# Kernel tuning notes

Measured on AMD Instinct MI355X. Metric: run time of the kernel, lower is better.

## Reference

```python
import jax, jax.numpy as jnp
import numpy as np
import math

WS = 8          # window size
DIM = 32        # per-head dim
NH = 8          # num_head
TH = 16         # total_head
B, H, W = 4, 128, 128
WA = WS * WS    # window area


def _rel_pos_index():
    coords = np.stack(np.meshgrid(np.arange(WS), np.arange(WS), indexing='ij'))  # (2, WS, WS)
    cf = coords.reshape(2, -1)                      # (2, WA)
    rc = cf[:, :, None] - cf[:, None, :]            # (2, WA, WA)
    rc = rc.transpose(1, 2, 0).copy()               # (WA, WA, 2)
    rc[:, :, 0] += WS - 1
    rc[:, :, 1] += WS - 1
    rc[:, :, 0] *= 2 * WS - 1
    return rc.sum(-1)                               # (WA, WA)


def setup_inputs() -> dict:
    key = jax.random.key(0)
    k1, k2, k3, k4 = jax.random.split(key, 4)
    qkv = jax.random.normal(k1, (B, NH, 3 * DIM, H, W), dtype=jnp.float32)
    ch = jax.random.normal(k2, (B, (TH - NH) * DIM, H, W), dtype=jnp.float32)
    logit_scale = jnp.log(10.0) * jnp.ones((NH, 1, 1), dtype=jnp.float32)
    rel_bias_table = 0.02 * jax.random.normal(k3, ((2 * WS - 1) ** 2, NH), dtype=jnp.float32)
    proj_w = 0.02 * jax.random.normal(k4, (NH * DIM, NH * DIM), dtype=jnp.float32)  # 1x1 conv
    proj_b = jnp.zeros((NH * DIM,), dtype=jnp.float32)
    rel_index = jnp.asarray(_rel_pos_index(), dtype=jnp.int32)
    return {"qkv": qkv, "ch": ch, "logit_scale": logit_scale,
            "rel_bias_table": rel_bias_table, "proj_w": proj_w,
            "proj_b": proj_b, "rel_index": rel_index}


def _window_partition(x):
    # x: (B, l, c, H, W) -> (B*nh*nw, l, WA, c)
    b, l, c, h, w = x.shape
    nh, nw = h // WS, w // WS
    x = x.reshape(b, l, c, nh, WS, nw, WS)
    x = x.transpose(0, 3, 5, 1, 4, 6, 2)            # b, nh, nw, l, wh, ww, c
    return x.reshape(b * nh * nw, l, WA, c)


def _l2norm(x):
    n = jnp.sqrt(jnp.sum(x * x, axis=-1, keepdims=True))
    return x / jnp.maximum(n, 1e-12)


def reference(qkv, ch, logit_scale, rel_bias_table, proj_w, proj_b, rel_index):
    b, L, C3, h, w = qkv.shape
    nh, nw = h // WS, w // WS
    qkvw = _window_partition(qkv)                   # (Bw, L, WA, 3*DIM)
    q, k, v = jnp.split(qkvw, 3, axis=-1)           # each (Bw, L, WA, DIM)

    # helper gating
    lch = TH - NH
    chw = _window_partition(ch.reshape(b, lch, DIM, h, w))  # (Bw, lch, WA, DIM)
    chm = jnp.mean(chw, axis=1, keepdims=True)      # (Bw, 1, WA, DIM)
    v = v * chm

    # cosine attention
    attn = jnp.einsum('wlqc,wlkc->wlqk', _l2norm(q), _l2norm(k))
    scale = jnp.exp(jnp.minimum(logit_scale, math.log(1.0 / 0.01)))  # (L,1,1)
    bias = rel_bias_table[rel_index.reshape(-1)].reshape(WA, WA, NH)
    bias = bias.transpose(2, 0, 1)[None]            # (1, L, WA, WA)
    attn = jax.nn.softmax(attn * scale[None] + bias, axis=-1)
    x = jnp.einsum('wlqk,wlkc->wlqc', attn, v)      # (Bw, L, WA, DIM)

    # window unpartition -> (B, L*DIM, H, W)
    x = x.reshape(b, nh, nw, L, WS, WS, DIM)
    x = x.transpose(0, 3, 6, 1, 4, 2, 5)            # b, l, c, nh, wh, nw, ww
    x = x.reshape(b, L * DIM, h, w)

    # 1x1 conv projection
    x = jnp.einsum('bchw,oc->bohw', x, proj_w) + proj_b[None, :, None, None]
    return x
```

## Files before the change

### kernel.cpp

```cpp
#include <hip/hip_runtime.h>


typedef __attribute__((ext_vector_type(8))) short short8v;
typedef __attribute__((ext_vector_type(4))) float f32x4;
typedef __attribute__((ext_vector_type(2))) unsigned int u32x2;

#define PLANE 16384

static __device__ __forceinline__ unsigned short f2bf(float x) {
  union { float f; unsigned u; } v; v.f = x;
  unsigned r = v.u + 0x7fff + ((v.u >> 16) & 1);
  return (unsigned short)(r >> 16);
}
static __device__ __forceinline__ float bf2f(unsigned short b) {
  union { unsigned u; float f; } v; v.u = ((unsigned)b) << 16;
  return v.f;
}

__global__ __launch_bounds__(256) void prep_kernel(
    const float* __restrict__ btab, const int* __restrict__ ridx,
    const float* __restrict__ pw, float* __restrict__ biasG,
    unsigned int* __restrict__ wbf)
{
  const int blk = blockIdx.x, tid = threadIdx.x;
  if (blk < 128) {
    int i = blk * 256 + tid;
    int h = i >> 12, qk = i & 4095;
    biasG[i] = btab[ridx[qk] * 8 + h];
  } else {
    int i = (blk - 128) * 256 + tid;
    wbf[i] = (unsigned)f2bf(pw[2 * i]) | ((unsigned)f2bf(pw[2 * i + 1]) << 16);
  }
}

__global__ __launch_bounds__(512, 4) void fused_kernel(
    const float* __restrict__ qkv, const float* __restrict__ ch,
    const float* __restrict__ lsc, const float* __restrict__ biasG,
    const unsigned short* __restrict__ wbf, const float* __restrict__ pb,
    float* __restrict__ out)
{
  __shared__ __align__(16) char smem[65536];
  float* chm = (float*)smem;

  const int tid = threadIdx.x;
  int bid = blockIdx.x;
  bid = (bid & 7) * 64 + (bid >> 3);
  const int b   = bid >> 7;
  const int wy  = (bid >> 3) & 15;
  const int wxp = bid & 7;
  const int y0  = wy << 3, x0 = wxp << 4;

  const int h = tid >> 6, lane = tid & 63;
  const int lg = lane >> 4, lr = lane & 15;

  {
    const float* cb = ch + ((size_t)(b * 256)) * PLANE;
#pragma unroll
    for (int t = 0; t < 2; ++t) {
      int idx = tid + t * 512;
      int c = idx >> 5, row = (idx >> 2) & 7, xq = idx & 3;
      const float4* src = (const float4*)(cb + (size_t)c * PLANE
                                          + (y0 + row) * 128 + x0) + xq;
      float4 a = {0.f, 0.f, 0.f, 0.f};
#pragma unroll
      for (int l = 0; l < 8; ++l) {
        float4 tv = src[(size_t)(l * 32) * (PLANE / 4)];
        a.x += tv.x; a.y += tv.y; a.z += tv.z; a.w += tv.w;
      }
      a.x *= 0.125f; a.y *= 0.125f; a.z *= 0.125f; a.w *= 0.125f;
      *(float4*)(chm + 132 * c + 16 * row + 4 * xq) = a;
    }
  }
  __syncthreads();

  const size_t qbase = ((size_t)((b * 8 + h) * 96)) * PLANE;
  const float* qg = qkv + qbase;
  const float* kg = qg + (size_t)32 * PLANE;
  const float* vg = qg + (size_t)64 * PLANE;
  const float scale = __expf(fminf(lsc[h], 4.6051701859880914f));

  short8v vf[2][2][2];
#pragma unroll
  for (int win = 0; win < 2; ++win) {
    const int xw = x0 + win * 8;
#pragma unroll
    for (int dt = 0; dt < 2; ++dt) {
      const int d = 16 * dt + lr;
      const float* vp = vg + (size_t)d * PLANE;
      const float* cm = chm + 132 * d;
#pragma unroll
      for (int m = 0; m < 2; ++m) {
        int ka = 4 * lg + 32 * m, kb2 = ka + 16;
        int ra = ka >> 3, ca = ka & 7, rb = kb2 >> 3, cb2 = kb2 & 7;
        float4 va  = *(const float4*)(vp + (y0 + ra) * 128 + xw + ca);
        float4 vb  = *(const float4*)(vp + (y0 + rb) * 128 + xw + cb2);
        f32x4 caf = *(const f32x4*)(cm + 16 * ra + 8 * win + ca);
        f32x4 cbf = *(const f32x4*)(cm + 16 * rb + 8 * win + cb2);
        vf[win][dt][m][0] = (short)f2bf(va.x * caf[0]);
        vf[win][dt][m][1] = (short)f2bf(va.y * caf[1]);
        vf[win][dt][m][2] = (short)f2bf(va.z * caf[2]);
        vf[win][dt][m][3] = (short)f2bf(va.w * caf[3]);
        vf[win][dt][m][4] = (short)f2bf(vb.x * cbf[0]);
        vf[win][dt][m][5] = (short)f2bf(vb.y * cbf[1]);
        vf[win][dt][m][6] = (short)f2bf(vb.z * cbf[2]);
        vf[win][dt][m][7] = (short)f2bf(vb.w * cbf[3]);
      }
    }
  }
  __syncthreads();

  const float* bgh = biasG + (h << 12);

#pragma unroll 1
  for (int win = 0; win < 2; ++win) {
    const int xw = x0 + win * 8;

    short8v khi[4], klo[4];
#pragma unroll
    for (int kt = 0; kt < 4; ++kt) {
      int kpos = 16 * kt + lr;
      int spk = (y0 + (kpos >> 3)) * 128 + xw + (kpos & 7);
      float kk[8], nr = 0.f;
#pragma unroll
      for (int j = 0; j < 8; ++j) {
        kk[j] = kg[(size_t)(8 * lg + j) * PLANE + spk];
        nr = fmaf(kk[j], kk[j], nr);
      }
      nr += __shfl_xor(nr, 16);
      nr += __shfl_xor(nr, 32);
      float iv = 1.f / fmaxf(sqrtf(nr), 1e-12f);
#pragma unroll
      for (int j = 0; j < 8; ++j) {
        float x = kk[j] * iv;
        unsigned short hb = f2bf(x);
        khi[kt][j] = (short)hb;
        klo[kt][j] = (short)f2bf(x - bf2f(hb));
      }
    }

#pragma unroll 1
    for (int st = 0; st < 4; ++st) {
      int q = 16 * st + lr;
      int spq = (y0 + (q >> 3)) * 128 + xw + (q & 7);
      float qq[8], nrq = 0.f;
#pragma unroll
      for (int j = 0; j < 8; ++j) {
        qq[j] = qg[(size_t)(8 * lg + j) * PLANE + spq];
        nrq = fmaf(qq[j], qq[j], nrq);
      }
      nrq += __shfl_xor(nrq, 16);
      nrq += __shfl_xor(nrq, 32);
      const float fq = scale / fmaxf(sqrtf(nrq), 1e-12f);

      short8v qhi, qlo;
#pragma unroll
      for (int j = 0; j < 8; ++j) {
        float x = qq[j] * fq;
        unsigned short hb = f2bf(x);
        qhi[j] = (short)hb;
        qlo[j] = (short)f2bf(x - bf2f(hb));
      }

      const float4* bq = (const float4*)(bgh + (q << 6));
      float e[16], mx = -1e30f;
#pragma unroll
      for (int kt = 0; kt < 4; ++kt) {
        f32x4 a = {0.f, 0.f, 0.f, 0.f};
        a = __builtin_amdgcn_mfma_f32_16x16x32_bf16(klo[kt], qhi, a, 0, 0, 0);
        a = __builtin_amdgcn_mfma_f32_16x16x32_bf16(khi[kt], qlo, a, 0, 0, 0);
        a = __builtin_amdgcn_mfma_f32_16x16x32_bf16(khi[kt], qhi, a, 0, 0, 0);
        float4 b4 = bq[4 * kt + lg];
        float bb[4] = {b4.x, b4.y, b4.z, b4.w};
#pragma unroll
        for (int r = 0; r < 4; ++r) {
          float lv = a[r] + bb[r];
          e[4 * kt + r] = lv;
          mx = fmaxf(mx, lv);
        }
      }
      mx = fmaxf(mx, __shfl_xor(mx, 16));
      mx = fmaxf(mx, __shfl_xor(mx, 32));
      float s = 0.f;
#pragma unroll
      for (int i = 0; i < 16; ++i) { e[i] = __expf(e[i] - mx); s += e[i]; }
      s += __shfl_xor(s, 16);
      s += __shfl_xor(s, 32);
      float rl = 1.f / s;

      short8v pf[2];
#pragma unroll
      for (int m = 0; m < 2; ++m)
#pragma unroll
        for (int j = 0; j < 8; ++j)
          pf[m][j] = (short)f2bf(e[4 * (j >> 2) + 8 * m + (j & 3)]);

      int pl = ((q >> 3) << 4) + win * 8 + (q & 7);
#pragma unroll
      for (int dt = 0; dt < 2; ++dt) {
        f32x4 o = {0.f, 0.f, 0.f, 0.f};
        o = __builtin_amdgcn_mfma_f32_16x16x32_bf16(vf[win][dt][0], pf[0], o, 0, 0, 0);
        o = __builtin_amdgcn_mfma_f32_16x16x32_bf16(vf[win][dt][1], pf[1], o, 0, 0, 0);
        u32x2 ww;
        ww[0] = (unsigned)f2bf(o[0] * rl) | ((unsigned)f2bf(o[1] * rl) << 16);
        ww[1] = (unsigned)f2bf(o[2] * rl) | ((unsigned)f2bf(o[3] * rl) << 16);
        unsigned off = (unsigned)(pl * 512)
                     + (((unsigned)(64 * h + 32 * dt + 8 * lg)) ^ ((unsigned)(pl & 7) << 4));
        *(u32x2*)(smem + off) = ww;
      }
    }
  }
  __syncthreads();

  f32x4 acc[2][8];
#pragma unroll
  for (int i = 0; i < 2; ++i)
#pragma unroll
    for (int j = 0; j < 8; ++j) acc[i][j] = (f32x4){0.f, 0.f, 0.f, 0.f};

#pragma unroll 1
  for (int kc = 0; kc < 8; ++kc) {
    short8v wf0 = *(const short8v*)(wbf + (size_t)(32 * h + lr) * 256 + 32 * kc + 8 * lg);
    short8v wf1 = *(const short8v*)(wbf + (size_t)(32 * h + 16 + lr) * 256 + 32 * kc + 8 * lg);
    short8v xf[8];
#pragma unroll
    for (int pt = 0; pt < 8; ++pt) {
      int pl = 16 * pt + lr;
      unsigned off = (unsigned)(pl * 512)
                   + (((unsigned)(64 * kc + 16 * lg)) ^ ((unsigned)(pl & 7) << 4));
      xf[pt] = *(const short8v*)(smem + off);
    }
#pragma unroll
    for (int pt = 0; pt < 8; ++pt) {
      acc[0][pt] = __builtin_amdgcn_mfma_f32_16x16x32_bf16(wf0, xf[pt], acc[0][pt], 0, 0, 0);
      acc[1][pt] = __builtin_amdgcn_mfma_f32_16x16x32_bf16(wf1, xf[pt], acc[1][pt], 0, 0, 0);
    }
  }

#pragma unroll
  for (int ot = 0; ot < 2; ++ot) {
#pragma unroll
    for (int r = 0; r < 4; ++r) {
      int o = 32 * h + 16 * ot + 4 * lg + r;
      float bv = pb[o];
      float* op = out + ((size_t)(b * 256 + o)) * PLANE;
#pragma unroll
      for (int pt = 0; pt < 8; ++pt)
        op[(y0 + pt) * 128 + x0 + lr] = acc[ot][pt][r] + bv;
    }
  }
}

extern "C" void kernel_launch(void* const* d_in, const int* in_sizes, int n_in,
                              void* d_out, int out_size, void* d_ws, size_t ws_size,
                              hipStream_t stream) {
  const float* qkv  = (const float*)d_in[0];
  const float* ch   = (const float*)d_in[1];
  const float* lsc  = (const float*)d_in[2];
  const float* btab = (const float*)d_in[3];
  const float* pw   = (const float*)d_in[4];
  const float* pb   = (const float*)d_in[5];
  const int*   ridx = (const int*)d_in[6];
  float* out = (float*)d_out;

  char* ws = (char*)d_ws;
  float*          biasG = (float*)ws;
  unsigned short* wbf   = (unsigned short*)(ws + 131072);

  prep_kernel<<<dim3(256), dim3(256), 0, stream>>>(btab, ridx, pw,
                                                   biasG, (unsigned int*)wbf);
  fused_kernel<<<dim3(512), dim3(512), 0, stream>>>(qkv, ch, lsc, biasG,
                                                    wbf, pb, out);
}
```

Baseline: 130.8 us.

## Remap waves to window/query tiles, loop heads with LDS-staged K and prefetch

Waves are reassigned from one attention head each to one (window, query-tile) pair each, and every wave now loops over all 8 heads. Each head's K tile is staged once per block into LDS as a bf16 hi/lo split, and the next head's K is prefetched into registers while the current head is processed. L2 normalisation of q and k is moved to a scale applied to the MFMA output instead of being applied to the inputs. The trade is two extra barriers per head, a larger LDS footprint, and four waves each reloading the same V and bias data, with slightly different rounding.

```diff
diff --git a/kernel.cpp b/kernel.cpp
--- a/kernel.cpp
+++ b/kernel.cpp
@@ -6,6 +6,7 @@
 typedef __attribute__((ext_vector_type(2))) unsigned int u32x2;
 
 #define PLANE 16384
+#define LOG100 4.6051701859880914f
 
 static __device__ __forceinline__ unsigned short f2bf(float x) {
   union { float f; unsigned u; } v; v.f = x;
@@ -39,8 +40,10 @@
     const unsigned short* __restrict__ wbf, const float* __restrict__ pb,
     float* __restrict__ out)
 {
-  __shared__ __align__(16) char smem[65536];
+  __shared__ __align__(16) char smem[81920];
   float* chm = (float*)smem;
+  unsigned short* sKhi = (unsigned short*)(smem + 65536);
+  unsigned short* sKlo = (unsigned short*)(smem + 73728);
 
   const int tid = threadIdx.x;
   int bid = blockIdx.x;
@@ -50,8 +53,10 @@
   const int wxp = bid & 7;
   const int y0  = wy << 3, x0 = wxp << 4;
 
-  const int h = tid >> 6, lane = tid & 63;
+  const int wv = tid >> 6, lane = tid & 63;
   const int lg = lane >> 4, lr = lane & 15;
+  const int win = wv >> 2, st = wv & 3;
+  const int xw  = x0 + win * 8;
 
   {
     const float* cb = ch + ((size_t)(b * 256)) * PLANE;
@@ -73,143 +78,171 @@
   }
   __syncthreads();
 
-  const size_t qbase = ((size_t)((b * 8 + h) * 96)) * PLANE;
-  const float* qg = qkv + qbase;
-  const float* kg = qg + (size_t)32 * PLANE;
-  const float* vg = qg + (size_t)64 * PLANE;
-  const float scale = __expf(fminf(lsc[h], 4.6051701859880914f));
-
-  short8v vf[2][2][2];
-#pragma unroll
-  for (int win = 0; win < 2; ++win) {
-    const int xw = x0 + win * 8;
+  unsigned cpk[2][2][4];
+#pragma unroll
+  for (int dt = 0; dt < 2; ++dt) {
+    const float* cm = chm + 132 * (16 * dt + lr);
+#pragma unroll
+    for (int m = 0; m < 2; ++m) {
+      int ka = 4 * lg + 32 * m, kb = ka + 16;
+      int pa = 16 * (ka >> 3) + 8 * win + (ka & 7);
+      int pb2 = 16 * (kb >> 3) + 8 * win + (kb & 7);
+      f32x4 ca = *(const f32x4*)(cm + pa);
+      f32x4 cb2 = *(const f32x4*)(cm + pb2);
+      cpk[dt][m][0] = (unsigned)f2bf(ca[0]) | ((unsigned)f2bf(ca[1]) << 16);
+      cpk[dt][m][1] = (unsigned)f2bf(ca[2]) | ((unsigned)f2bf(ca[3]) << 16);
+      cpk[dt][m][2] = (unsigned)f2bf(cb2[0]) | ((unsigned)f2bf(cb2[1]) << 16);
+      cpk[dt][m][3] = (unsigned)f2bf(cb2[2]) | ((unsigned)f2bf(cb2[3]) << 16);
+    }
+  }
+  __syncthreads();
+
+  const int sq4 = tid & 3;
+  const int sdd = ((tid >> 2) & 15) | ((tid >> 8) << 4);
+  const int sr2 = (tid >> 6) & 3;
+  const int sgo1 = (y0 + sr2) * 128 + x0 + 4 * sq4;
+  const int sgo2 = (y0 + sr2 + 4) * 128 + x0 + 4 * sq4;
+  const int sp1 = 16 * sr2 + 4 * sq4;
+  const int sp2 = 16 * (sr2 + 4) + 4 * sq4;
+
+  const size_t qkv0 = ((size_t)(b * 8) * 96) * PLANE;
+  const float* kg0 = qkv + qkv0 + (size_t)(32 + sdd) * PLANE;
+
+  float4 f1 = *(const float4*)(kg0 + sgo1);
+  float4 f2 = *(const float4*)(kg0 + sgo2);
+
+#pragma unroll 1
+  for (int h = 0; h < 8; ++h) {
+    {
+#define STG(val, pos_) { unsigned short hb_ = f2bf(val);                     \
+        sKhi[32 * (pos_) + sdd] = hb_;                                       \
+        sKlo[32 * (pos_) + sdd] = f2bf((val) - bf2f(hb_)); }
+      STG(f1.x, sp1 + 0) STG(f1.y, sp1 + 1) STG(f1.z, sp1 + 2) STG(f1.w, sp1 + 3)
+      STG(f2.x, sp2 + 0) STG(f2.y, sp2 + 1) STG(f2.z, sp2 + 2) STG(f2.w, sp2 + 3)
+#undef STG
+    }
+    __syncthreads();
+
+    if (h < 7) {
+      const float* kgn = qkv + qkv0 + (size_t)((h + 1) * 96 + 32 + sdd) * PLANE;
+      f1 = *(const float4*)(kgn + sgo1);
+      f2 = *(const float4*)(kgn + sgo2);
+    }
+
+    const float* qg = qkv + qkv0 + (size_t)(h * 96) * PLANE;
+    const float* vg = qg + (size_t)64 * PLANE;
+    const float scale = __expf(fminf(lsc[h], LOG100));
+    const int q = 16 * st + lr;
+    const int spq = (y0 + (q >> 3)) * 128 + xw + (q & 7);
+
+    float qq[8];
+#pragma unroll
+    for (int j = 0; j < 8; ++j)
+      qq[j] = qg[(size_t)(8 * lg + j) * PLANE + spq];
+
+    short8v vf[2][2];
 #pragma unroll
     for (int dt = 0; dt < 2; ++dt) {
-      const int d = 16 * dt + lr;
-      const float* vp = vg + (size_t)d * PLANE;
-      const float* cm = chm + 132 * d;
+      const float* vp = vg + (size_t)(16 * dt + lr) * PLANE;
 #pragma unroll
       for (int m = 0; m < 2; ++m) {
-        int ka = 4 * lg + 32 * m, kb2 = ka + 16;
-        int ra = ka >> 3, ca = ka & 7, rb = kb2 >> 3, cb2 = kb2 & 7;
-        float4 va  = *(const float4*)(vp + (y0 + ra) * 128 + xw + ca);
-        float4 vb  = *(const float4*)(vp + (y0 + rb) * 128 + xw + cb2);
-        f32x4 caf = *(const f32x4*)(cm + 16 * ra + 8 * win + ca);
-        f32x4 cbf = *(const f32x4*)(cm + 16 * rb + 8 * win + cb2);
-        vf[win][dt][m][0] = (short)f2bf(va.x * caf[0]);
-        vf[win][dt][m][1] = (short)f2bf(va.y * caf[1]);
-        vf[win][dt][m][2] = (short)f2bf(va.z * caf[2]);
-        vf[win][dt][m][3] = (short)f2bf(va.w * caf[3]);
-        vf[win][dt][m][4] = (short)f2bf(vb.x * cbf[0]);
-        vf[win][dt][m][5] = (short)f2bf(vb.y * cbf[1]);
-        vf[win][dt][m][6] = (short)f2bf(vb.z * cbf[2]);
-        vf[win][dt][m][7] = (short)f2bf(vb.w * cbf[3]);
+        int ka = 4 * lg + 32 * m, kb = ka + 16;
+        float4 va = *(const float4*)(vp + (y0 + (ka >> 3)) * 128 + xw + (ka & 7));
+        float4 vb = *(const float4*)(vp + (y0 + (kb >> 3)) * 128 + xw + (kb & 7));
+        const unsigned* cp = cpk[dt][m];
+        vf[dt][m][0] = (short)f2bf(va.x * bf2f((unsigned short)(cp[0] & 0xffff)));
+        vf[dt][m][1] = (short)f2bf(va.y * bf2f((unsigned short)(cp[0] >> 16)));
+        vf[dt][m][2] = (short)f2bf(va.z * bf2f((unsigned short)(cp[1] & 0xffff)));
+        vf[dt][m][3] = (short)f2bf(va.w * bf2f((unsigned short)(cp[1] >> 16)));
+        vf[dt][m][4] = (short)f2bf(vb.x * bf2f((unsigned short)(cp[2] & 0xffff)));
+        vf[dt][m][5] = (short)f2bf(vb.y * bf2f((unsigned short)(cp[2] >> 16)));
+        vf[dt][m][6] = (short)f2bf(vb.z * bf2f((unsigned short)(cp[3] & 0xffff)));
+        vf[dt][m][7] = (short)f2bf(vb.w * bf2f((unsigned short)(cp[3] >> 16)));
       }
     }
-  }
-  __syncthreads();
-
-  const float* bgh = biasG + (h << 12);
-
-#pragma unroll 1
-  for (int win = 0; win < 2; ++win) {
-    const int xw = x0 + win * 8;
 
     short8v khi[4], klo[4];
+    float ivk[4];
 #pragma unroll
     for (int kt = 0; kt < 4; ++kt) {
-      int kpos = 16 * kt + lr;
-      int spk = (y0 + (kpos >> 3)) * 128 + xw + (kpos & 7);
-      float kk[8], nr = 0.f;
+      int pp = 16 * (2 * kt + (lr >> 3)) + 8 * win + (lr & 7);
+      khi[kt] = *(const short8v*)(sKhi + 32 * pp + 8 * lg);
+      klo[kt] = *(const short8v*)(sKlo + 32 * pp + 8 * lg);
+      float nr = 0.f;
 #pragma unroll
       for (int j = 0; j < 8; ++j) {
-        kk[j] = kg[(size_t)(8 * lg + j) * PLANE + spk];
-        nr = fmaf(kk[j], kk[j], nr);
+        float kr = bf2f((unsigned short)khi[kt][j]) + bf2f((unsigned short)klo[kt][j]);
+        nr = fmaf(kr, kr, nr);
       }
       nr += __shfl_xor(nr, 16);
       nr += __shfl_xor(nr, 32);
-      float iv = 1.f / fmaxf(sqrtf(nr), 1e-12f);
-#pragma unroll
-      for (int j = 0; j < 8; ++j) {
-        float x = kk[j] * iv;
-        unsigned short hb = f2bf(x);
-        khi[kt][j] = (short)hb;
-        klo[kt][j] = (short)f2bf(x - bf2f(hb));
+      ivk[kt] = 1.f / fmaxf(sqrtf(nr), 1e-12f);
+    }
+
+    float nrq = 0.f;
+#pragma unroll
+    for (int j = 0; j < 8; ++j) nrq = fmaf(qq[j], qq[j], nrq);
+    nrq += __shfl_xor(nrq, 16);
+    nrq += __shfl_xor(nrq, 32);
+    const float fq = scale / fmaxf(sqrtf(nrq), 1e-12f);
+
+    short8v qhi, qlo;
+#pragma unroll
+    for (int j = 0; j < 8; ++j) {
+      unsigned short hb = f2bf(qq[j]);
+      qhi[j] = (short)hb;
+      qlo[j] = (short)f2bf(qq[j] - bf2f(hb));
+    }
+
+    const float4* bq = (const float4*)(biasG + (h << 12) + (q << 6));
+    float e[16], mx = -1e30f;
+#pragma unroll
+    for (int kt = 0; kt < 4; ++kt) {
+      f32x4 a = {0.f, 0.f, 0.f, 0.f};
+      a = __builtin_amdgcn_mfma_f32_16x16x32_bf16(klo[kt], qhi, a, 0, 0, 0);
+      a = __builtin_amdgcn_mfma_f32_16x16x32_bf16(khi[kt], qlo, a, 0, 0, 0);
+      a = __builtin_amdgcn_mfma_f32_16x16x32_bf16(khi[kt], qhi, a, 0, 0, 0);
+      float4 b4 = bq[4 * kt + lg];
+      float bb[4] = {b4.x, b4.y, b4.z, b4.w};
+#pragma unroll
+      for (int r = 0; r < 4; ++r) {
+        float fkr = __shfl(ivk[kt], 4 * lg + r);
+        float lv = a[r] * (fq * fkr) + bb[r];
+        e[4 * kt + r] = lv;
+        mx = fmaxf(mx, lv);
       }
     }
-
-#pragma unroll 1
-    for (int st = 0; st < 4; ++st) {
-      int q = 16 * st + lr;
-      int spq = (y0 + (q >> 3)) * 128 + xw + (q & 7);
-      float qq[8], nrq = 0.f;
-#pragma unroll
-      for (int j = 0; j < 8; ++j) {
-        qq[j] = qg[(size_t)(8 * lg + j) * PLANE + spq];
-        nrq = fmaf(qq[j], qq[j], nrq);
-      }
-      nrq += __shfl_xor(nrq, 16);
-      nrq += __shfl_xor(nrq, 32);
-      const float fq = scale / fmaxf(sqrtf(nrq), 1e-12f);
-
-      short8v qhi, qlo;
-#pragma unroll
-      for (int j = 0; j < 8; ++j) {
-        float x = qq[j] * fq;
-        unsigned short hb = f2bf(x);
-        qhi[j] = (short)hb;
-        qlo[j] = (short)f2bf(x - bf2f(hb));
-      }
-
-      const float4* bq = (const float4*)(bgh + (q << 6));
-      float e[16], mx = -1e30f;
-#pragma unroll
-      for (int kt = 0; kt < 4; ++kt) {
-        f32x4 a = {0.f, 0.f, 0.f, 0.f};
-        a = __builtin_amdgcn_mfma_f32_16x16x32_bf16(klo[kt], qhi, a, 0, 0, 0);
-        a = __builtin_amdgcn_mfma_f32_16x16x32_bf16(khi[kt], qlo, a, 0, 0, 0);
-        a = __builtin_amdgcn_mfma_f32_16x16x32_bf16(khi[kt], qhi, a, 0, 0, 0);
-        float4 b4 = bq[4 * kt + lg];
-        float bb[4] = {b4.x, b4.y, b4.z, b4.w};
-#pragma unroll
-        for (int r = 0; r < 4; ++r) {
-          float lv = a[r] + bb[r];
-          e[4 * kt + r] = lv;
-          mx = fmaxf(mx, lv);
-        }
-      }
-      mx = fmaxf(mx, __shfl_xor(mx, 16));
-      mx = fmaxf(mx, __shfl_xor(mx, 32));
-      float s = 0.f;
-#pragma unroll
-      for (int i = 0; i < 16; ++i) { e[i] = __expf(e[i] - mx); s += e[i]; }
-      s += __shfl_xor(s, 16);
-      s += __shfl_xor(s, 32);
-      float rl = 1.f / s;
-
-      short8v pf[2];
-#pragma unroll
-      for (int m = 0; m < 2; ++m)
-#pragma unroll
-        for (int j = 0; j < 8; ++j)
-          pf[m][j] = (short)f2bf(e[4 * (j >> 2) + 8 * m + (j & 3)]);
-
-      int pl = ((q >> 3) << 4) + win * 8 + (q & 7);
-#pragma unroll
-      for (int dt = 0; dt < 2; ++dt) {
-        f32x4 o = {0.f, 0.f, 0.f, 0.f};
-        o = __builtin_amdgcn_mfma_f32_16x16x32_bf16(vf[win][dt][0], pf[0], o, 0, 0, 0);
-        o = __builtin_amdgcn_mfma_f32_16x16x32_bf16(vf[win][dt][1], pf[1], o, 0, 0, 0);
-        u32x2 ww;
-        ww[0] = (unsigned)f2bf(o[0] * rl) | ((unsigned)f2bf(o[1] * rl) << 16);
-        ww[1] = (unsigned)f2bf(o[2] * rl) | ((unsigned)f2bf(o[3] * rl) << 16);
-        unsigned off = (unsigned)(pl * 512)
-                     + (((unsigned)(64 * h + 32 * dt + 8 * lg)) ^ ((unsigned)(pl & 7) << 4));
-        *(u32x2*)(smem + off) = ww;
-      }
-    }
-  }
-  __syncthreads();
+    mx = fmaxf(mx, __shfl_xor(mx, 16));
+    mx = fmaxf(mx, __shfl_xor(mx, 32));
+    float s = 0.f;
+#pragma unroll
+    for (int i = 0; i < 16; ++i) { e[i] = __expf(e[i] - mx); s += e[i]; }
+    s += __shfl_xor(s, 16);
+    s += __shfl_xor(s, 32);
+    float rl = 1.f / s;
+
+    short8v pf[2];
+#pragma unroll
+    for (int m = 0; m < 2; ++m)
+#pragma unroll
+      for (int j = 0; j < 8; ++j)
+        pf[m][j] = (short)f2bf(e[4 * (j >> 2) + 8 * m + (j & 3)]);
+
+    int pl = ((q >> 3) << 4) + win * 8 + (q & 7);
+#pragma unroll
+    for (int dt = 0; dt < 2; ++dt) {
+      f32x4 o = {0.f, 0.f, 0.f, 0.f};
+      o = __builtin_amdgcn_mfma_f32_16x16x32_bf16(vf[dt][0], pf[0], o, 0, 0, 0);
+      o = __builtin_amdgcn_mfma_f32_16x16x32_bf16(vf[dt][1], pf[1], o, 0, 0, 0);
+      u32x2 ww;
+      ww[0] = (unsigned)f2bf(o[0] * rl) | ((unsigned)f2bf(o[1] * rl) << 16);
+      ww[1] = (unsigned)f2bf(o[2] * rl) | ((unsigned)f2bf(o[3] * rl) << 16);
+      unsigned off = (unsigned)(pl * 512)
+                   + (((unsigned)(64 * h + 32 * dt + 8 * lg)) ^ ((unsigned)(pl & 7) << 4));
+      *(u32x2*)(smem + off) = ww;
+    }
+    __syncthreads();
+  }
 
   f32x4 acc[2][8];
 #pragma unroll
@@ -219,8 +252,8 @@
 
 #pragma unroll 1
   for (int kc = 0; kc < 8; ++kc) {
-    short8v wf0 = *(const short8v*)(wbf + (size_t)(32 * h + lr) * 256 + 32 * kc + 8 * lg);
-    short8v wf1 = *(const short8v*)(wbf + (size_t)(32 * h + 16 + lr) * 256 + 32 * kc + 8 * lg);
+    short8v wf0 = *(const short8v*)(wbf + (size_t)(32 * wv + lr) * 256 + 32 * kc + 8 * lg);
+    short8v wf1 = *(const short8v*)(wbf + (size_t)(32 * wv + 16 + lr) * 256 + 32 * kc + 8 * lg);
     short8v xf[8];
 #pragma unroll
     for (int pt = 0; pt < 8; ++pt) {
@@ -240,7 +273,7 @@
   for (int ot = 0; ot < 2; ++ot) {
 #pragma unroll
     for (int r = 0; r < 4; ++r) {
-      int o = 32 * h + 16 * ot + 4 * lg + r;
+      int o = 32 * wv + 16 * ot + 4 * lg + r;
       float bv = pb[o];
       float* op = out + ((size_t)(b * 256 + o)) * PLANE;
 #pragma unroll
```

Result: slower. 176.2 us (+34.6%).

## Double block to 1024 threads, one wave per head-window, prefetch loads

Applied to the files above, without the earlier changes.

The fused kernel now launches 1024 threads per block, so each wave handles a single (head, window) pair instead of looping over two windows, and the projection GEMM is split across twice as many waves. Q, K and V global loads are issued up front, before the helper-mean reduction and the barrier, so their latency overlaps that reduction. The chm buffer moves to its own LDS region, making shared memory about 80KB, and register pressure rises from holding all q/k values at once. Occupancy limits from the larger block and LDS could offset the extra parallelism.

```diff
diff --git a/kernel.cpp b/kernel.cpp
--- a/kernel.cpp
+++ b/kernel.cpp
@@ -6,6 +6,7 @@
 typedef __attribute__((ext_vector_type(2))) unsigned int u32x2;
 
 #define PLANE 16384
+#define LOG100 4.6051701859880914f
 
 static __device__ __forceinline__ unsigned short f2bf(float x) {
   union { float f; unsigned u; } v; v.f = x;
@@ -33,14 +34,14 @@
   }
 }
 
-__global__ __launch_bounds__(512, 4) void fused_kernel(
+__global__ __launch_bounds__(1024, 4) void fused_kernel(
     const float* __restrict__ qkv, const float* __restrict__ ch,
     const float* __restrict__ lsc, const float* __restrict__ biasG,
     const unsigned short* __restrict__ wbf, const float* __restrict__ pb,
     float* __restrict__ out)
 {
-  __shared__ __align__(16) char smem[65536];
-  float* chm = (float*)smem;
+  __shared__ __align__(16) char smem[82432];
+  float* chm = (float*)(smem + 65536);
 
   const int tid = threadIdx.x;
   int bid = blockIdx.x;
@@ -50,187 +51,193 @@
   const int wxp = bid & 7;
   const int y0  = wy << 3, x0 = wxp << 4;
 
-  const int h = tid >> 6, lane = tid & 63;
+  const int wv = tid >> 6, lane = tid & 63;
   const int lg = lane >> 4, lr = lane & 15;
-
-  {
-    const float* cb = ch + ((size_t)(b * 256)) * PLANE;
-#pragma unroll
-    for (int t = 0; t < 2; ++t) {
-      int idx = tid + t * 512;
-      int c = idx >> 5, row = (idx >> 2) & 7, xq = idx & 3;
-      const float4* src = (const float4*)(cb + (size_t)c * PLANE
-                                          + (y0 + row) * 128 + x0) + xq;
-      float4 a = {0.f, 0.f, 0.f, 0.f};
-#pragma unroll
-      for (int l = 0; l < 8; ++l) {
-        float4 tv = src[(size_t)(l * 32) * (PLANE / 4)];
-        a.x += tv.x; a.y += tv.y; a.z += tv.z; a.w += tv.w;
-      }
-      a.x *= 0.125f; a.y *= 0.125f; a.z *= 0.125f; a.w *= 0.125f;
-      *(float4*)(chm + 132 * c + 16 * row + 4 * xq) = a;
-    }
-  }
-  __syncthreads();
+  const int h = wv & 7, win = wv >> 3;
+  const int xw = x0 + win * 8;
 
   const size_t qbase = ((size_t)((b * 8 + h) * 96)) * PLANE;
   const float* qg = qkv + qbase;
   const float* kg = qg + (size_t)32 * PLANE;
   const float* vg = qg + (size_t)64 * PLANE;
-  const float scale = __expf(fminf(lsc[h], 4.6051701859880914f));
-
-  short8v vf[2][2][2];
-#pragma unroll
-  for (int win = 0; win < 2; ++win) {
-    const int xw = x0 + win * 8;
+
+  float4 vA[2][2], vB[2][2];
+#pragma unroll
+  for (int dt = 0; dt < 2; ++dt) {
+    const float* vp = vg + (size_t)(16 * dt + lr) * PLANE;
+#pragma unroll
+    for (int m = 0; m < 2; ++m) {
+      int ka = 4 * lg + 32 * m, kb = ka + 16;
+      vA[dt][m] = *(const float4*)(vp + (y0 + (ka >> 3)) * 128 + xw + (ka & 7));
+      vB[dt][m] = *(const float4*)(vp + (y0 + (kb >> 3)) * 128 + xw + (kb & 7));
+    }
+  }
+  float kk[4][8];
+#pragma unroll
+  for (int kt = 0; kt < 4; ++kt) {
+    int kpos = 16 * kt + lr;
+    int spk = (y0 + (kpos >> 3)) * 128 + xw + (kpos & 7);
+#pragma unroll
+    for (int j = 0; j < 8; ++j)
+      kk[kt][j] = kg[(size_t)(8 * lg + j) * PLANE + spk];
+  }
+  float qq[4][8];
+#pragma unroll
+  for (int st = 0; st < 4; ++st) {
+    int q = 16 * st + lr;
+    int spq = (y0 + (q >> 3)) * 128 + xw + (q & 7);
+#pragma unroll
+    for (int j = 0; j < 8; ++j)
+      qq[st][j] = qg[(size_t)(8 * lg + j) * PLANE + spq];
+  }
+
+  {
+    const float* cb = ch + ((size_t)(b * 256)) * PLANE;
+    int c = tid >> 5, row = (tid >> 2) & 7, xq = tid & 3;
+    const float4* src = (const float4*)(cb + (size_t)c * PLANE
+                                        + (y0 + row) * 128 + x0) + xq;
+    float4 a = {0.f, 0.f, 0.f, 0.f};
+#pragma unroll
+    for (int l = 0; l < 8; ++l) {
+      float4 tv = src[(size_t)(l * 32) * (PLANE / 4)];
+      a.x += tv.x; a.y += tv.y; a.z += tv.z; a.w += tv.w;
+    }
+    a.x *= 0.125f; a.y *= 0.125f; a.z *= 0.125f; a.w *= 0.125f;
+    *(float4*)(chm + 132 * c + 16 * row + 4 * xq) = a;
+  }
+  __syncthreads();
+
+  const float scale = __expf(fminf(lsc[h], LOG100));
+
+  short8v vf[2][2];
+#pragma unroll
+  for (int dt = 0; dt < 2; ++dt) {
+    const float* cm = chm + 132 * (16 * dt + lr);
+#pragma unroll
+    for (int m = 0; m < 2; ++m) {
+      int ka = 4 * lg + 32 * m, kb = ka + 16;
+      f32x4 caf = *(const f32x4*)(cm + 16 * (ka >> 3) + 8 * win + (ka & 7));
+      f32x4 cbf = *(const f32x4*)(cm + 16 * (kb >> 3) + 8 * win + (kb & 7));
+      float4 va = vA[dt][m], vb = vB[dt][m];
+      vf[dt][m][0] = (short)f2bf(va.x * caf[0]);
+      vf[dt][m][1] = (short)f2bf(va.y * caf[1]);
+      vf[dt][m][2] = (short)f2bf(va.z * caf[2]);
+      vf[dt][m][3] = (short)f2bf(va.w * caf[3]);
+      vf[dt][m][4] = (short)f2bf(vb.x * cbf[0]);
+      vf[dt][m][5] = (short)f2bf(vb.y * cbf[1]);
+      vf[dt][m][6] = (short)f2bf(vb.z * cbf[2]);
+      vf[dt][m][7] = (short)f2bf(vb.w * cbf[3]);
+    }
+  }
+
+  short8v khi[4], klo[4];
+#pragma unroll
+  for (int kt = 0; kt < 4; ++kt) {
+    float nr = 0.f;
+#pragma unroll
+    for (int j = 0; j < 8; ++j) nr = fmaf(kk[kt][j], kk[kt][j], nr);
+    nr += __shfl_xor(nr, 16);
+    nr += __shfl_xor(nr, 32);
+    float iv = 1.f / fmaxf(sqrtf(nr), 1e-12f);
+#pragma unroll
+    for (int j = 0; j < 8; ++j) {
+      float x = kk[kt][j] * iv;
+      unsigned short hb = f2bf(x);
+      khi[kt][j] = (short)hb;
+      klo[kt][j] = (short)f2bf(x - bf2f(hb));
+    }
+  }
+
+#pragma unroll
+  for (int st = 0; st < 4; ++st) {
+    const int q = 16 * st + lr;
+
+    float nrq = 0.f;
+#pragma unroll
+    for (int j = 0; j < 8; ++j) nrq = fmaf(qq[st][j], qq[st][j], nrq);
+    nrq += __shfl_xor(nrq, 16);
+    nrq += __shfl_xor(nrq, 32);
+    const float fq = scale / fmaxf(sqrtf(nrq), 1e-12f);
+
+    short8v qhi, qlo;
+#pragma unroll
+    for (int j = 0; j < 8; ++j) {
+      float x = qq[st][j] * fq;
+      unsigned short hb = f2bf(x);
+      qhi[j] = (short)hb;
+      qlo[j] = (short)f2bf(x - bf2f(hb));
+    }
+
+    const float4* bq = (const float4*)(biasG + (h << 12) + (q << 6));
+    float e[16], mx = -1e30f;
+#pragma unroll
+    for (int kt = 0; kt < 4; ++kt) {
+      f32x4 a = {0.f, 0.f, 0.f, 0.f};
+      a = __builtin_amdgcn_mfma_f32_16x16x32_bf16(klo[kt], qhi, a, 0, 0, 0);
+      a = __builtin_amdgcn_mfma_f32_16x16x32_bf16(khi[kt], qlo, a, 0, 0, 0);
+      a = __builtin_amdgcn_mfma_f32_16x16x32_bf16(khi[kt], qhi, a, 0, 0, 0);
+      float4 b4 = bq[4 * kt + lg];
+      float bb[4] = {b4.x, b4.y, b4.z, b4.w};
+#pragma unroll
+      for (int r = 0; r < 4; ++r) {
+        float lv = a[r] + bb[r];
+        e[4 * kt + r] = lv;
+        mx = fmaxf(mx, lv);
+      }
+    }
+    mx = fmaxf(mx, __shfl_xor(mx, 16));
+    mx = fmaxf(mx, __shfl_xor(mx, 32));
+    float s = 0.f;
+#pragma unroll
+    for (int i = 0; i < 16; ++i) { e[i] = __expf(e[i] - mx); s += e[i]; }
+    s += __shfl_xor(s, 16);
+    s += __shfl_xor(s, 32);
+    float rl = 1.f / s;
+
+    short8v pf[2];
+#pragma unroll
+    for (int m = 0; m < 2; ++m)
+#pragma unroll
+      for (int j = 0; j < 8; ++j)
+        pf[m][j] = (short)f2bf(e[4 * (j >> 2) + 8 * m + (j & 3)]);
+
+    int pl = ((q >> 3) << 4) + win * 8 + (q & 7);
 #pragma unroll
     for (int dt = 0; dt < 2; ++dt) {
-      const int d = 16 * dt + lr;
-      const float* vp = vg + (size_t)d * PLANE;
-      const float* cm = chm + 132 * d;
-#pragma unroll
-      for (int m = 0; m < 2; ++m) {
-        int ka = 4 * lg + 32 * m, kb2 = ka + 16;
-        int ra = ka >> 3, ca = ka & 7, rb = kb2 >> 3, cb2 = kb2 & 7;
-        float4 va  = *(const float4*)(vp + (y0 + ra) * 128 + xw + ca);
-        float4 vb  = *(const float4*)(vp + (y0 + rb) * 128 + xw + cb2);
-        f32x4 caf = *(const f32x4*)(cm + 16 * ra + 8 * win + ca);
-        f32x4 cbf = *(const f32x4*)(cm + 16 * rb + 8 * win + cb2);
-        vf[win][dt][m][0] = (short)f2bf(va.x * caf[0]);
-        vf[win][dt][m][1] = (short)f2bf(va.y * caf[1]);
-        vf[win][dt][m][2] = (short)f2bf(va.z * caf[2]);
-        vf[win][dt][m][3] = (short)f2bf(va.w * caf[3]);
-        vf[win][dt][m][4] = (short)f2bf(vb.x * cbf[0]);
-        vf[win][dt][m][5] = (short)f2bf(vb.y * cbf[1]);
-        vf[win][dt][m][6] = (short)f2bf(vb.z * cbf[2]);
-        vf[win][dt][m][7] = (short)f2bf(vb.w * cbf[3]);
-      }
+      f32x4 o = {0.f, 0.f, 0.f, 0.f};
+      o = __builtin_amdgcn_mfma_f32_16x16x32_bf16(vf[dt][0], pf[0], o, 0, 0, 0);
+      o = __builtin_amdgcn_mfma_f32_16x16x32_bf16(vf[dt][1], pf[1], o, 0, 0, 0);
+      u32x2 ww;
+      ww[0] = (unsigned)f2bf(o[0] * rl) | ((unsigned)f2bf(o[1] * rl) << 16);
+      ww[1] = (unsigned)f2bf(o[2] * rl) | ((unsigned)f2bf(o[3] * rl) << 16);
+      unsigned off = (unsigned)(pl * 512)
+                   + (((unsigned)(64 * h + 32 * dt + 8 * lg)) ^ ((unsigned)(pl & 7) << 4));
+      *(u32x2*)(smem + off) = ww;
     }
   }
   __syncthreads();
 
-  const float* bgh = biasG + (h << 12);
-
-#pragma unroll 1
-  for (int win = 0; win < 2; ++win) {
-    const int xw = x0 + win * 8;
-
-    short8v khi[4], klo[4];
-#pragma unroll
-    for (int kt = 0; kt < 4; ++kt) {
-      int kpos = 16 * kt + lr;
-      int spk = (y0 + (kpos >> 3)) * 128 + xw + (kpos & 7);
-      float kk[8], nr = 0.f;
-#pragma unroll
-      for (int j = 0; j < 8; ++j) {
-        kk[j] = kg[(size_t)(8 * lg + j) * PLANE + spk];
-        nr = fmaf(kk[j], kk[j], nr);
-      }
-      nr += __shfl_xor(nr, 16);
-      nr += __shfl_xor(nr, 32);
-      float iv = 1.f / fmaxf(sqrtf(nr), 1e-12f);
-#pragma unroll
-      for (int j = 0; j < 8; ++j) {
-        float x = kk[j] * iv;
-        unsigned short hb = f2bf(x);
-        khi[kt][j] = (short)hb;
-        klo[kt][j] = (short)f2bf(x - bf2f(hb));
-      }
-    }
-
-#pragma unroll 1
-    for (int st = 0; st < 4; ++st) {
-      int q = 16 * st + lr;
-      int spq = (y0 + (q >> 3)) * 128 + xw + (q & 7);
-      float qq[8], nrq = 0.f;
-#pragma unroll
-      for (int j = 0; j < 8; ++j) {
-        qq[j] = qg[(size_t)(8 * lg + j) * PLANE + spq];
-        nrq = fmaf(qq[j], qq[j], nrq);
-      }
-      nrq += __shfl_xor(nrq, 16);
-      nrq += __shfl_xor(nrq, 32);
-      const float fq = scale / fmaxf(sqrtf(nrq), 1e-12f);
-
-      short8v qhi, qlo;
-#pragma unroll
-      for (int j = 0; j < 8; ++j) {
-        float x = qq[j] * fq;
-        unsigned short hb = f2bf(x);
-        qhi[j] = (short)hb;
-        qlo[j] = (short)f2bf(x - bf2f(hb));
-      }
-
-      const float4* bq = (const float4*)(bgh + (q << 6));
-      float e[16], mx = -1e30f;
-#pragma unroll
-      for (int kt = 0; kt < 4; ++kt) {
-        f32x4 a = {0.f, 0.f, 0.f, 0.f};
-        a = __builtin_amdgcn_mfma_f32_16x16x32_bf16(klo[kt], qhi, a, 0, 0, 0);
-        a = __builtin_amdgcn_mfma_f32_16x16x32_bf16(khi[kt], qlo, a, 0, 0, 0);
-        a = __builtin_amdgcn_mfma_f32_16x16x32_bf16(khi[kt], qhi, a, 0, 0, 0);
-        float4 b4 = bq[4 * kt + lg];
-        float bb[4] = {b4.x, b4.y, b4.z, b4.w};
-#pragma unroll
-        for (int r = 0; r < 4; ++r) {
-          float lv = a[r] + bb[r];
-          e[4 * kt + r] = lv;
-          mx = fmaxf(mx, lv);
-        }
-      }
-      mx = fmaxf(mx, __shfl_xor(mx, 16));
-      mx = fmaxf(mx, __shfl_xor(mx, 32));
-      float s = 0.f;
-#pragma unroll
-      for (int i = 0; i < 16; ++i) { e[i] = __expf(e[i] - mx); s += e[i]; }
-      s += __shfl_xor(s, 16);
-      s += __shfl_xor(s, 32);
-      float rl = 1.f / s;
-
-      short8v pf[2];
-#pragma unroll
-      for (int m = 0; m < 2; ++m)
-#pragma unroll
-        for (int j = 0; j < 8; ++j)
-          pf[m][j] = (short)f2bf(e[4 * (j >> 2) + 8 * m + (j & 3)]);
-
-      int pl = ((q >> 3) << 4) + win * 8 + (q & 7);
-#pragma unroll
-      for (int dt = 0; dt < 2; ++dt) {
-        f32x4 o = {0.f, 0.f, 0.f, 0.f};
-        o = __builtin_amdgcn_mfma_f32_16x16x32_bf16(vf[win][dt][0], pf[0], o, 0, 0, 0);
-        o = __builtin_amdgcn_mfma_f32_16x16x32_bf16(vf[win][dt][1], pf[1], o, 0, 0, 0);
-        u32x2 ww;
-        ww[0] = (unsigned)f2bf(o[0] * rl) | ((unsigned)f2bf(o[1] * rl) << 16);
-        ww[1] = (unsigned)f2bf(o[2] * rl) | ((unsigned)f2bf(o[3] * rl) << 16);
-        unsigned off = (unsigned)(pl * 512)
-                     + (((unsigned)(64 * h + 32 * dt + 8 * lg)) ^ ((unsigned)(pl & 7) << 4));
-        *(u32x2*)(smem + off) = ww;
-      }
-    }
-  }
-  __syncthreads();
-
-  f32x4 acc[2][8];
+  const int ow = wv & 7, ph = wv >> 3;
+  f32x4 acc[2][4];
 #pragma unroll
   for (int i = 0; i < 2; ++i)
 #pragma unroll
-    for (int j = 0; j < 8; ++j) acc[i][j] = (f32x4){0.f, 0.f, 0.f, 0.f};
-
-#pragma unroll 1
+    for (int j = 0; j < 4; ++j) acc[i][j] = (f32x4){0.f, 0.f, 0.f, 0.f};
+
+#pragma unroll
   for (int kc = 0; kc < 8; ++kc) {
-    short8v wf0 = *(const short8v*)(wbf + (size_t)(32 * h + lr) * 256 + 32 * kc + 8 * lg);
-    short8v wf1 = *(const short8v*)(wbf + (size_t)(32 * h + 16 + lr) * 256 + 32 * kc + 8 * lg);
-    short8v xf[8];
-#pragma unroll
-    for (int pt = 0; pt < 8; ++pt) {
-      int pl = 16 * pt + lr;
+    short8v wf0 = *(const short8v*)(wbf + (size_t)(32 * ow + lr) * 256 + 32 * kc + 8 * lg);
+    short8v wf1 = *(const short8v*)(wbf + (size_t)(32 * ow + 16 + lr) * 256 + 32 * kc + 8 * lg);
+    short8v xf[4];
+#pragma unroll
+    for (int pt = 0; pt < 4; ++pt) {
+      int pl = 64 * ph + 16 * pt + lr;
       unsigned off = (unsigned)(pl * 512)
                    + (((unsigned)(64 * kc + 16 * lg)) ^ ((unsigned)(pl & 7) << 4));
       xf[pt] = *(const short8v*)(smem + off);
     }
 #pragma unroll
-    for (int pt = 0; pt < 8; ++pt) {
+    for (int pt = 0; pt < 4; ++pt) {
       acc[0][pt] = __builtin_amdgcn_mfma_f32_16x16x32_bf16(wf0, xf[pt], acc[0][pt], 0, 0, 0);
       acc[1][pt] = __builtin_amdgcn_mfma_f32_16x16x32_bf16(wf1, xf[pt], acc[1][pt], 0, 0, 0);
     }
@@ -240,12 +247,12 @@
   for (int ot = 0; ot < 2; ++ot) {
 #pragma unroll
     for (int r = 0; r < 4; ++r) {
-      int o = 32 * h + 16 * ot + 4 * lg + r;
+      int o = 32 * ow + 16 * ot + 4 * lg + r;
       float bv = pb[o];
       float* op = out + ((size_t)(b * 256 + o)) * PLANE;
 #pragma unroll
-      for (int pt = 0; pt < 8; ++pt)
-        op[(y0 + pt) * 128 + x0 + lr] = acc[ot][pt][r] + bv;
+      for (int pt = 0; pt < 4; ++pt)
+        op[(y0 + 4 * ph + pt) * 128 + x0 + lr] = acc[ot][pt][r] + bv;
     }
   }
 }
@@ -268,6 +275,6 @@
 
   prep_kernel<<<dim3(256), dim3(256), 0, stream>>>(btab, ridx, pw,
                                                    biasG, (unsigned int*)wbf);
-  fused_kernel<<<dim3(512), dim3(512), 0, stream>>>(qkv, ch, lsc, biasG,
-                                                    wbf, pb, out);
-}
+  fused_kernel<<<dim3(512), dim3(1024), 0, stream>>>(qkv, ch, lsc, biasG,
+                                                     wbf, pb, out);
+}
```

Result: slower. 197.0 us (+50.6%).
